# Optimization experiments

Hardware: AMD Instinct MI355X
Metric: run time of the kernel (lower is better)

The kernel has to match this reference:

```python
import jax, jax.numpy as jnp
import numpy as np

B, L, D, H, C, V, NC = 64, 64, 300, 128, 50, 50000, 2
LAMDA = 0.1
KS = (3, 4, 5)


def setup_inputs() -> dict:
    key = jax.random.key(0)
    ks = jax.random.split(key, 16)
    n = lambda k, shp, s=0.02: (jax.random.normal(k, shp, jnp.float32) * s)
    return {
        "x": jax.random.randint(ks[0], (B, L), 0, V),
        "embedmatrix": n(ks[1], (V, D), 0.1),
        "att_w1a": n(ks[2], (D, H)),      # first half of attlinear1 weight (for curembed)
        "att_w1b": n(ks[3], (D, H)),      # second half (for the paired embedding)
        "att_b1": jnp.zeros((H,), jnp.float32),
        "att_w2": n(ks[4], (H,)),
        "att_b2": jnp.zeros((), jnp.float32),
        "conv_w1": n(ks[5], (C, 2 * D, KS[0])), "conv_b1": jnp.zeros((C,), jnp.float32),
        "conv_w2": n(ks[6], (C, 2 * D, KS[1])), "conv_b2": jnp.zeros((C,), jnp.float32),
        "conv_w3": n(ks[7], (C, 2 * D, KS[2])), "conv_b3": jnp.zeros((C,), jnp.float32),
        "lin_w": n(ks[8], (3 * C, NC)), "lin_b": jnp.zeros((NC,), jnp.float32),
    }


def _attention(emb, w1a, w1b, b1, w2, b2):
    # Faithful vectorization of attentionembed/attentionword, including the
    # original's use of the COMPACTED index for the score partner and decay.
    Bb, Ll, Dd = emb.shape
    pa = emb @ w1a                        # [B,L,H]  curembed projection
    pb = emb[:, : Ll - 1] @ w1b           # [B,L-1,H] partner is outputs[:, index]
    h = jnp.tanh(pa[:, :, None, :] + pb[:, None, :, :] + b1)  # [B,L,L-1,H]
    s = h @ w2 + b2                       # [B,L,L-1]
    i = jnp.arange(Ll)[:, None]
    k = jnp.arange(Ll - 1)[None, :]
    decay = (1.0 - LAMDA) ** (jnp.abs(i - k) - 1).astype(jnp.float32)  # [L,L-1]
    alpha = jax.nn.softmax(decay * s, axis=-1)                         # [B,L,L-1]
    # attended embeddings use j = k + (k >= i) (skip position i)
    idx = k + (k >= i)                    # [L,L-1]
    alpha_full = jnp.zeros((Bb, Ll, Ll), emb.dtype).at[:, i, idx].set(alpha)
    return jnp.einsum('blm,bmd->bld', alpha_full, emb)  # [B,L,D]


def reference(x, embedmatrix, att_w1a, att_w1b, att_b1, att_w2, att_b2,
              conv_w1, conv_b1, conv_w2, conv_b2, conv_w3, conv_b3,
              lin_w, lin_b):
    emb = embedmatrix[x]                                   # [B,L,D]
    att = _attention(emb, att_w1a, att_w1b, att_b1, att_w2, att_b2)
    feat = jnp.concatenate([emb, att], axis=2).transpose(0, 2, 1)  # [B,2D,L]
    pooled = []
    for w, b in ((conv_w1, conv_b1), (conv_w2, conv_b2), (conv_w3, conv_b3)):
        y = jax.lax.conv_general_dilated(
            feat, w, window_strides=(1,), padding='VALID',
            dimension_numbers=('NCH', 'OIH', 'NCH')) + b[None, :, None]
        pooled.append(jnp.max(y, axis=-1))                 # pool over full valid length -> [B,C]
    conout = jnp.concatenate(pooled, axis=1)               # [B,3C]; dropout is identity in eval
    logits = conout @ lin_w + lin_b                        # [B,NC]
    return jax.nn.log_softmax(logits, axis=1)
```

## Files before the change

kernel.cpp:

```cpp
#include <hip/hip_runtime.h>
#include <math.h>

#define B_ 64
#define L_ 64
#define D_ 300
#define H_ 128
#define TWO_D 600
#define M_ 4096
#define Q_ 600
#define KP 640
#define KPA 320
#define HH 256

typedef short short8 __attribute__((ext_vector_type(8)));
typedef float floatx4 __attribute__((ext_vector_type(4)));

static __device__ __forceinline__ unsigned short f2bf(float f) {
    unsigned int u = __float_as_uint(f);
    u += 0x7FFFu + ((u >> 16) & 1u);
    return (unsigned short)(u >> 16);
}
static __device__ __forceinline__ float fast_tanh(float x) {
    float e = __expf(2.0f * x);
    return 1.0f - 2.0f * __builtin_amdgcn_rcpf(e + 1.0f);
}

__global__ __launch_bounds__(256) void k_prep(const int* __restrict__ x, const float* __restrict__ em,
        const float* __restrict__ w1a, const float* __restrict__ w1b,
        const float* __restrict__ cw1, const float* __restrict__ cw2, const float* __restrict__ cw3,
        unsigned short* __restrict__ fvb, unsigned short* __restrict__ wtT,
        unsigned short* __restrict__ w1abT) {
    int blk = blockIdx.x, tid = threadIdx.x;
    if (blk < 512) {
        #pragma unroll
        for (int r = 0; r < 8; ++r) {
            int m = blk * 8 + r;
            const float* src = em + (size_t)x[m] * D_;
            unsigned short* dst = fvb + (size_t)m * KP;
            for (int d = tid; d < KPA; d += 256) dst[d] = (d < D_) ? f2bf(src[d]) : 0;
            if (tid < 40) dst[TWO_D + tid] = 0;
        }
    } else if (blk < 912) {
        int base = ((blk - 512) * 256 + tid) * 4;
        #pragma unroll
        for (int e = 0; e < 4; ++e) {
            int idx = base + e;
            int q = idx / KP, d = idx - q * KP;
            float v = 0.f;
            if (q < Q_ && d < TWO_D) {
                if (q < 150)      { int c = q/3, i = q%3;                 v = cw1[((size_t)c*TWO_D + d)*3 + i]; }
                else if (q < 350) { int r2 = q-150; int c = r2/4, i = r2%4; v = cw2[((size_t)c*TWO_D + d)*4 + i]; }
                else              { int r2 = q-350; int c = r2/5, i = r2%5; v = cw3[((size_t)c*TWO_D + d)*5 + i]; }
            }
            wtT[idx] = f2bf(v);
        }
    } else {
        int base = ((blk - 912) * 256 + tid) * 4;
        #pragma unroll
        for (int e = 0; e < 4; ++e) {
            int idx = base + e;
            int h = idx / KPA, d = idx - h * KPA;
            float v = 0.f;
            if (d < D_) v = (h < H_) ? w1a[(size_t)d * H_ + h] : w1b[(size_t)d * H_ + (h - H_)];
            w1abT[idx] = f2bf(v);
        }
    }
}

__global__ __launch_bounds__(256) void k_papb(const unsigned short* __restrict__ A,
                                              const unsigned short* __restrict__ Bt,
                                              const float* __restrict__ b1,
                                              float* __restrict__ pab) {
    __shared__ unsigned short sA[64 * 72];
    __shared__ unsigned short sB[64 * 72];
    int m0 = blockIdx.x * 64, n0 = blockIdx.y * 64;
    int tid = threadIdx.x, lane = tid & 63, wave = tid >> 6;
    int wr = wave >> 1, wc = wave & 1;
    int sr = tid >> 2, so = (tid & 3) * 16;
    floatx4 acc[2][2] = {};
    int lr = lane & 15, lk = (lane >> 4) * 8;
    for (int k0 = 0; k0 < KPA; k0 += 64) {
        const unsigned short* Ar = &A [(size_t)(m0 + sr) * KP  + k0 + so];
        const unsigned short* Br = &Bt[(size_t)(n0 + sr) * KPA + k0 + so];
        *(uint4*)&sA[sr * 72 + so]     = *(const uint4*)Ar;
        *(uint4*)&sA[sr * 72 + so + 8] = *(const uint4*)(Ar + 8);
        *(uint4*)&sB[sr * 72 + so]     = *(const uint4*)Br;
        *(uint4*)&sB[sr * 72 + so + 8] = *(const uint4*)(Br + 8);
        __syncthreads();
        #pragma unroll
        for (int kk = 0; kk < 64; kk += 32) {
            short8 a0 = *(const short8*)&sA[(wr * 32 +  0 + lr) * 72 + kk + lk];
            short8 a1 = *(const short8*)&sA[(wr * 32 + 16 + lr) * 72 + kk + lk];
            short8 b0 = *(const short8*)&sB[(wc * 32 +  0 + lr) * 72 + kk + lk];
            short8 b1 = *(const short8*)&sB[(wc * 32 + 16 + lr) * 72 + kk + lk];
            acc[0][0] = __builtin_amdgcn_mfma_f32_16x16x32_bf16(a0, b0, acc[0][0], 0, 0, 0);
            acc[0][1] = __builtin_amdgcn_mfma_f32_16x16x32_bf16(a0, b1, acc[0][1], 0, 0, 0);
            acc[1][0] = __builtin_amdgcn_mfma_f32_16x16x32_bf16(a1, b0, acc[1][0], 0, 0, 0);
            acc[1][1] = __builtin_amdgcn_mfma_f32_16x16x32_bf16(a1, b1, acc[1][1], 0, 0, 0);
        }
        __syncthreads();
    }
    int drow = (lane >> 4) * 4, dcol = lane & 15;
    #pragma unroll
    for (int mi = 0; mi < 2; ++mi)
        #pragma unroll
        for (int ni = 0; ni < 2; ++ni) {
            int col = n0 + wc * 32 + ni * 16 + dcol;
            float bias = (col < H_) ? b1[col] : 0.f;
            #pragma unroll
            for (int i = 0; i < 4; ++i) {
                int row = m0 + wr * 32 + mi * 16 + drow + i;
                pab[(size_t)row * HH + col] = acc[mi][ni][i] + bias;
            }
        }
}

#define AT_PITCH 132
__global__ __launch_bounds__(256) void k_attn(const float* __restrict__ pab,
                                              const float* __restrict__ w2g,
                                              const float* __restrict__ b2,
                                              unsigned short* __restrict__ af) {
    int blk = blockIdx.x;
    int b = blk >> 2;
    int i0 = (blk & 3) * 16;
    __shared__ float pbL[64 * AT_PITCH];
    __shared__ float paL[16 * 128];
    __shared__ float s_w2[128];
    int tid = threadIdx.x, wave = tid >> 6, lane = tid & 63;
    {
        int r = tid >> 2, c0 = (tid & 3) * 32;
        #pragma unroll
        for (int c = 0; c < 32; c += 4) {
            float4 v = *(const float4*)&pab[(size_t)(b * 64 + r) * HH + H_ + c0 + c];
            *(float4*)&pbL[r * AT_PITCH + c0 + c] = v;
        }
    }
    {
        int idx = tid * 8;
        int ri = idx >> 7, h = idx & 127;
        const float* src = &pab[(size_t)(b * 64 + i0 + ri) * HH + h];
        *(float4*)&paL[idx]     = *(const float4*)src;
        *(float4*)&paL[idx + 4] = *(const float4*)(src + 4);
    }
    if (tid < 128) s_w2[tid] = w2g[tid];
    __syncthreads();

    float b2v = b2[0];
    int k = lane;
    float p0 = 0.f, p1 = 0.f, p2 = 0.f, p3 = 0.f;
    const float* pbrow = &pbL[k * AT_PITCH];
    const float* par = &paL[(wave * 4) * 128];
    for (int h = 0; h < 128; h += 4) {
        float4 pb4 = *(const float4*)&pbrow[h];
        float4 w4  = *(const float4*)&s_w2[h];
        float4 a0  = *(const float4*)&par[h];
        float4 a1  = *(const float4*)&par[128 + h];
        float4 a2  = *(const float4*)&par[256 + h];
        float4 a3  = *(const float4*)&par[384 + h];
        p0 += w4.x * fast_tanh(a0.x + pb4.x) + w4.y * fast_tanh(a0.y + pb4.y)
            + w4.z * fast_tanh(a0.z + pb4.z) + w4.w * fast_tanh(a0.w + pb4.w);
        p1 += w4.x * fast_tanh(a1.x + pb4.x) + w4.y * fast_tanh(a1.y + pb4.y)
            + w4.z * fast_tanh(a1.z + pb4.z) + w4.w * fast_tanh(a1.w + pb4.w);
        p2 += w4.x * fast_tanh(a2.x + pb4.x) + w4.y * fast_tanh(a2.y + pb4.y)
            + w4.z * fast_tanh(a2.z + pb4.z) + w4.w * fast_tanh(a2.w + pb4.w);
        p3 += w4.x * fast_tanh(a3.x + pb4.x) + w4.y * fast_tanh(a3.y + pb4.y)
            + w4.z * fast_tanh(a3.z + pb4.z) + w4.w * fast_tanh(a3.w + pb4.w);
    }
    #pragma unroll
    for (int j = 0; j < 4; ++j) {
        float p = (j == 0) ? p0 : (j == 1) ? p1 : (j == 2) ? p2 : p3;
        int i = i0 + wave * 4 + j;
        p += b2v;
        float v;
        if (k < 63) {
            float e = fabsf((float)(i - k)) - 1.0f;
            v = __expf(e * -0.10536051565782628f) * p;
        } else v = -INFINITY;
        float mx = v;
        #pragma unroll
        for (int off = 32; off; off >>= 1) mx = fmaxf(mx, __shfl_xor(mx, off, 64));
        float ex = (k < 63) ? __expf(v - mx) : 0.f;
        float sm = ex;
        #pragma unroll
        for (int off = 32; off; off >>= 1) sm += __shfl_xor(sm, off, 64);
        float alpha = ex * __builtin_amdgcn_rcpf(sm);
        int jj = (k < 63) ? (k + (k >= i)) : i;
        af[(size_t)(b * 64 + i) * 64 + jj] = (k < 63) ? f2bf(alpha) : (unsigned short)0;
    }
}

__global__ __launch_bounds__(256) void k_att_mfma(const unsigned short* __restrict__ af,
                                                  unsigned short* __restrict__ fvb) {
    int b = blockIdx.x;
    int n0 = blockIdx.y * 64;
    __shared__ unsigned short sA[64 * 72];
    __shared__ unsigned short sBt[64 * 72];
    int tid = threadIdx.x, wave = tid >> 6, lane = tid & 63;
    int sr = tid >> 2, so = (tid & 3) * 16;
    *(uint4*)&sA[sr * 72 + so]     = *(const uint4*)&af[(size_t)(b * 64 + sr) * 64 + so];
    *(uint4*)&sA[sr * 72 + so + 8] = *(const uint4*)&af[(size_t)(b * 64 + sr) * 64 + so + 8];
    int dg = n0 + lane;
    #pragma unroll
    for (int p = 0; p < 16; ++p) {
        int m = p * 4 + wave;
        unsigned short v = (dg < D_) ? fvb[(size_t)(b * 64 + m) * KP + dg] : (unsigned short)0;
        sBt[lane * 72 + m] = v;
    }
    __syncthreads();
    int wr = wave >> 1, wc = wave & 1;
    int lr = lane & 15, lk = (lane >> 4) * 8;
    floatx4 acc[2][2] = {};
    #pragma unroll
    for (int k0 = 0; k0 < 64; k0 += 32) {
        short8 a0 = *(const short8*)&sA [(wr * 32 +  0 + lr) * 72 + k0 + lk];
        short8 a1 = *(const short8*)&sA [(wr * 32 + 16 + lr) * 72 + k0 + lk];
        short8 b0 = *(const short8*)&sBt[(wc * 32 +  0 + lr) * 72 + k0 + lk];
        short8 b1 = *(const short8*)&sBt[(wc * 32 + 16 + lr) * 72 + k0 + lk];
        acc[0][0] = __builtin_amdgcn_mfma_f32_16x16x32_bf16(a0, b0, acc[0][0], 0, 0, 0);
        acc[0][1] = __builtin_amdgcn_mfma_f32_16x16x32_bf16(a0, b1, acc[0][1], 0, 0, 0);
        acc[1][0] = __builtin_amdgcn_mfma_f32_16x16x32_bf16(a1, b0, acc[1][0], 0, 0, 0);
        acc[1][1] = __builtin_amdgcn_mfma_f32_16x16x32_bf16(a1, b1, acc[1][1], 0, 0, 0);
    }
    int drow = (lane >> 4) * 4, dcol = lane & 15;
    #pragma unroll
    for (int mi = 0; mi < 2; ++mi)
        #pragma unroll
        for (int ni = 0; ni < 2; ++ni) {
            int dgo = n0 + wc * 32 + ni * 16 + dcol;
            if (dgo >= D_) continue;
            #pragma unroll
            for (int i = 0; i < 4; ++i) {
                int row = wr * 32 + mi * 16 + drow + i;
                fvb[(size_t)(b * 64 + row) * KP + D_ + dgo] = f2bf(acc[mi][ni][i]);
            }
        }
}

__global__ __launch_bounds__(256) void k_gemmT(const unsigned short* __restrict__ Wt,
                                               const unsigned short* __restrict__ Bv,
                                               float* __restrict__ GT) {
    __shared__ unsigned short sA[64 * 72];
    __shared__ unsigned short sB[64 * 72];
    int q0 = blockIdx.x * 64, n0 = blockIdx.y * 64;
    int tid = threadIdx.x, lane = tid & 63, wave = tid >> 6;
    int wr = wave >> 1, wc = wave & 1;
    int sr = tid >> 2, so = (tid & 3) * 16;
    floatx4 acc[2][2] = {};
    int lr = lane & 15, lk = (lane >> 4) * 8;
    for (int k0 = 0; k0 < KP; k0 += 64) {
        const unsigned short* Ar = &Wt[(size_t)(q0 + sr) * KP + k0 + so];
        const unsigned short* Br = &Bv[(size_t)(n0 + sr) * KP + k0 + so];
        *(uint4*)&sA[sr * 72 + so]     = *(const uint4*)Ar;
        *(uint4*)&sA[sr * 72 + so + 8] = *(const uint4*)(Ar + 8);
        *(uint4*)&sB[sr * 72 + so]     = *(const uint4*)Br;
        *(uint4*)&sB[sr * 72 + so + 8] = *(const uint4*)(Br + 8);
        __syncthreads();
        #pragma unroll
        for (int kk = 0; kk < 64; kk += 32) {
            short8 a0 = *(const short8*)&sA[(wr * 32 +  0 + lr) * 72 + kk + lk];
            short8 a1 = *(const short8*)&sA[(wr * 32 + 16 + lr) * 72 + kk + lk];
            short8 b0 = *(const short8*)&sB[(wc * 32 +  0 + lr) * 72 + kk + lk];
            short8 b1 = *(const short8*)&sB[(wc * 32 + 16 + lr) * 72 + kk + lk];
            acc[0][0] = __builtin_amdgcn_mfma_f32_16x16x32_bf16(a0, b0, acc[0][0], 0, 0, 0);
            acc[0][1] = __builtin_amdgcn_mfma_f32_16x16x32_bf16(a0, b1, acc[0][1], 0, 0, 0);
            acc[1][0] = __builtin_amdgcn_mfma_f32_16x16x32_bf16(a1, b0, acc[1][0], 0, 0, 0);
            acc[1][1] = __builtin_amdgcn_mfma_f32_16x16x32_bf16(a1, b1, acc[1][1], 0, 0, 0);
        }
        __syncthreads();
    }
    int drow = (lane >> 4) * 4, dcol = lane & 15;
    #pragma unroll
    for (int mi = 0; mi < 2; ++mi)
        #pragma unroll
        for (int ni = 0; ni < 2; ++ni) {
            int qrow = q0 + wr * 32 + mi * 16 + drow;
            int col  = n0 + wc * 32 + ni * 16 + dcol;
            #pragma unroll
            for (int i = 0; i < 4; ++i)
                GT[(size_t)(qrow + i) * M_ + col] = acc[mi][ni][i];
        }
}

__global__ __launch_bounds__(256) void k_pool(const float* __restrict__ GT,
        const float* __restrict__ cb1, const float* __restrict__ cb2, const float* __restrict__ cb3,
        float* __restrict__ conout) {
    int task = blockIdx.x * 4 + (threadIdx.x >> 6);
    int lane = threadIdx.x & 63;
    int b = task / 150, p = task - b * 150;
    int ks, qb; float bias;
    if (p < 50)       { ks = 3; qb = p * 3;              bias = cb1[p]; }
    else if (p < 100) { int c = p - 50;  ks = 4; qb = 150 + c * 4; bias = cb2[c]; }
    else              { int c = p - 100; ks = 5; qb = 350 + c * 5; bias = cb3[c]; }
    int T = L_ - ks + 1;
    float y = -INFINITY;
    if (lane < T) {
        float s = bias;
        for (int i = 0; i < ks; ++i)
            s += GT[(size_t)(qb + i) * M_ + b * 64 + lane + i];
        y = s;
    }
    #pragma unroll
    for (int off = 32; off; off >>= 1) y = fmaxf(y, __shfl_xor(y, off, 64));
    if (lane == 0) conout[b * 150 + p] = y;
}

__global__ void k_final(const float* __restrict__ conout, const float* __restrict__ lw,
                        const float* __restrict__ lb, float* __restrict__ out) {
    int b = threadIdx.x;
    if (b >= B_) return;
    float l0 = lb[0], l1 = lb[1];
    const float* co = conout + b * 150;
    for (int m = 0; m < 150; ++m) {
        float v = co[m];
        l0 += v * lw[m * 2 + 0];
        l1 += v * lw[m * 2 + 1];
    }
    float mx = fmaxf(l0, l1);
    float ls = mx + logf(expf(l0 - mx) + expf(l1 - mx));
    out[b * 2 + 0] = l0 - ls;
    out[b * 2 + 1] = l1 - ls;
}

extern "C" void kernel_launch(void* const* d_in, const int* in_sizes, int n_in,
                              void* d_out, int out_size, void* d_ws, size_t ws_size,
                              hipStream_t stream) {
    const int*   x   = (const int*)  d_in[0];
    const float* em  = (const float*)d_in[1];
    const float* w1a = (const float*)d_in[2];
    const float* w1b = (const float*)d_in[3];
    const float* b1  = (const float*)d_in[4];
    const float* w2  = (const float*)d_in[5];
    const float* b2  = (const float*)d_in[6];
    const float* cw1 = (const float*)d_in[7];
    const float* cb1 = (const float*)d_in[8];
    const float* cw2 = (const float*)d_in[9];
    const float* cb2 = (const float*)d_in[10];
    const float* cw3 = (const float*)d_in[11];
    const float* cb3 = (const float*)d_in[12];
    const float* lw  = (const float*)d_in[13];
    const float* lb  = (const float*)d_in[14];
    float* out = (float*)d_out;

    float* ws = (float*)d_ws;
    float*          GT     = ws;
    unsigned short* af     = (unsigned short*)ws;
    float*          pab    = ws + 2621440;
    unsigned short* fvb    = (unsigned short*)(ws + 3670016);
    unsigned short* WtT    = (unsigned short*)(ws + 4980736);
    unsigned short* w1abT  = (unsigned short*)(ws + 5185536);
    float*          conout = ws + 5226496;

    hipLaunchKernelGGL(k_prep, dim3(992), dim3(256), 0, stream,
                       x, em, w1a, w1b, cw1, cw2, cw3, fvb, WtT, w1abT);
    hipLaunchKernelGGL(k_papb, dim3(M_ / 64, HH / 64), dim3(256), 0, stream,
                       fvb, w1abT, b1, pab);
    hipLaunchKernelGGL(k_attn, dim3(256), dim3(256), 0, stream, pab, w2, b2, af);
    hipLaunchKernelGGL(k_att_mfma, dim3(B_, 5), dim3(256), 0, stream, af, fvb);
    hipLaunchKernelGGL(k_gemmT, dim3(KP / 64, M_ / 64), dim3(256), 0, stream,
                       WtT, fvb, GT);
    hipLaunchKernelGGL(k_pool, dim3(2400), dim3(256), 0, stream,
                       GT, cb1, cb2, cb3, conout);
    hipLaunchKernelGGL(k_final, dim3(1), dim3(64), 0, stream, conout, lw, lb, out);
}
```

Baseline: 61.80 us.

## Fuse pooling with final linear, widen gemm tile, double attention block threads

Three changes. The pool and final-linear kernels are merged into one kernel per batch that max-pools each conv channel and accumulates the two logits through shared memory, which drops a launch and the conout round-trip. The transposed conv GEMM now computes 64x128 tiles with 8 MFMA accumulators per wave, halving the grid and reusing each A fragment across more columns. The attention-score kernel runs 512 threads with 2 query rows per wave instead of 4, doubling waves per block at the cost of more block-level parallel overhead.

```diff
diff --git a/kernel.cpp b/kernel.cpp
--- a/kernel.cpp
+++ b/kernel.cpp
@@ -116,7 +116,7 @@
 }
 
 #define AT_PITCH 132
-__global__ __launch_bounds__(256) void k_attn(const float* __restrict__ pab,
+__global__ __launch_bounds__(512) void k_attn(const float* __restrict__ pab,
                                               const float* __restrict__ w2g,
                                               const float* __restrict__ b2,
                                               unsigned short* __restrict__ af) {
@@ -128,48 +128,40 @@
     __shared__ float s_w2[128];
     int tid = threadIdx.x, wave = tid >> 6, lane = tid & 63;
     {
-        int r = tid >> 2, c0 = (tid & 3) * 32;
-        #pragma unroll
-        for (int c = 0; c < 32; c += 4) {
+        int r = tid >> 3, c0 = (tid & 7) * 16;
+        #pragma unroll
+        for (int c = 0; c < 16; c += 4) {
             float4 v = *(const float4*)&pab[(size_t)(b * 64 + r) * HH + H_ + c0 + c];
             *(float4*)&pbL[r * AT_PITCH + c0 + c] = v;
         }
     }
     {
-        int idx = tid * 8;
+        int idx = tid * 4;
         int ri = idx >> 7, h = idx & 127;
-        const float* src = &pab[(size_t)(b * 64 + i0 + ri) * HH + h];
-        *(float4*)&paL[idx]     = *(const float4*)src;
-        *(float4*)&paL[idx + 4] = *(const float4*)(src + 4);
+        *(float4*)&paL[idx] = *(const float4*)&pab[(size_t)(b * 64 + i0 + ri) * HH + h];
     }
     if (tid < 128) s_w2[tid] = w2g[tid];
     __syncthreads();
 
     float b2v = b2[0];
     int k = lane;
-    float p0 = 0.f, p1 = 0.f, p2 = 0.f, p3 = 0.f;
+    float p0 = 0.f, p1 = 0.f;
     const float* pbrow = &pbL[k * AT_PITCH];
-    const float* par = &paL[(wave * 4) * 128];
+    const float* par = &paL[(wave * 2) * 128];
     for (int h = 0; h < 128; h += 4) {
         float4 pb4 = *(const float4*)&pbrow[h];
         float4 w4  = *(const float4*)&s_w2[h];
         float4 a0  = *(const float4*)&par[h];
         float4 a1  = *(const float4*)&par[128 + h];
-        float4 a2  = *(const float4*)&par[256 + h];
-        float4 a3  = *(const float4*)&par[384 + h];
         p0 += w4.x * fast_tanh(a0.x + pb4.x) + w4.y * fast_tanh(a0.y + pb4.y)
             + w4.z * fast_tanh(a0.z + pb4.z) + w4.w * fast_tanh(a0.w + pb4.w);
         p1 += w4.x * fast_tanh(a1.x + pb4.x) + w4.y * fast_tanh(a1.y + pb4.y)
             + w4.z * fast_tanh(a1.z + pb4.z) + w4.w * fast_tanh(a1.w + pb4.w);
-        p2 += w4.x * fast_tanh(a2.x + pb4.x) + w4.y * fast_tanh(a2.y + pb4.y)
-            + w4.z * fast_tanh(a2.z + pb4.z) + w4.w * fast_tanh(a2.w + pb4.w);
-        p3 += w4.x * fast_tanh(a3.x + pb4.x) + w4.y * fast_tanh(a3.y + pb4.y)
-            + w4.z * fast_tanh(a3.z + pb4.z) + w4.w * fast_tanh(a3.w + pb4.w);
-    }
-    #pragma unroll
-    for (int j = 0; j < 4; ++j) {
-        float p = (j == 0) ? p0 : (j == 1) ? p1 : (j == 2) ? p2 : p3;
-        int i = i0 + wave * 4 + j;
+    }
+    #pragma unroll
+    for (int j = 0; j < 2; ++j) {
+        float p = (j == 0) ? p0 : p1;
+        int i = i0 + wave * 2 + j;
         p += b2v;
         float v;
         if (k < 63) {
@@ -240,85 +232,90 @@
                                                const unsigned short* __restrict__ Bv,
                                                float* __restrict__ GT) {
     __shared__ unsigned short sA[64 * 72];
-    __shared__ unsigned short sB[64 * 72];
-    int q0 = blockIdx.x * 64, n0 = blockIdx.y * 64;
+    __shared__ unsigned short sB[128 * 72];
+    int q0 = blockIdx.x * 64, n0 = blockIdx.y * 128;
     int tid = threadIdx.x, lane = tid & 63, wave = tid >> 6;
-    int wr = wave >> 1, wc = wave & 1;
-    int sr = tid >> 2, so = (tid & 3) * 16;
-    floatx4 acc[2][2] = {};
+    int srA = tid >> 2, soA = (tid & 3) * 16;
+    int srB = tid >> 1, soB = (tid & 1) * 32;
+    floatx4 acc[4][2] = {};
     int lr = lane & 15, lk = (lane >> 4) * 8;
     for (int k0 = 0; k0 < KP; k0 += 64) {
-        const unsigned short* Ar = &Wt[(size_t)(q0 + sr) * KP + k0 + so];
-        const unsigned short* Br = &Bv[(size_t)(n0 + sr) * KP + k0 + so];
-        *(uint4*)&sA[sr * 72 + so]     = *(const uint4*)Ar;
-        *(uint4*)&sA[sr * 72 + so + 8] = *(const uint4*)(Ar + 8);
-        *(uint4*)&sB[sr * 72 + so]     = *(const uint4*)Br;
-        *(uint4*)&sB[sr * 72 + so + 8] = *(const uint4*)(Br + 8);
+        const unsigned short* Ar = &Wt[(size_t)(q0 + srA) * KP + k0 + soA];
+        *(uint4*)&sA[srA * 72 + soA]     = *(const uint4*)Ar;
+        *(uint4*)&sA[srA * 72 + soA + 8] = *(const uint4*)(Ar + 8);
+        const unsigned short* Br = &Bv[(size_t)(n0 + srB) * KP + k0 + soB];
+        *(uint4*)&sB[srB * 72 + soB]      = *(const uint4*)Br;
+        *(uint4*)&sB[srB * 72 + soB + 8]  = *(const uint4*)(Br + 8);
+        *(uint4*)&sB[srB * 72 + soB + 16] = *(const uint4*)(Br + 16);
+        *(uint4*)&sB[srB * 72 + soB + 24] = *(const uint4*)(Br + 24);
         __syncthreads();
         #pragma unroll
         for (int kk = 0; kk < 64; kk += 32) {
-            short8 a0 = *(const short8*)&sA[(wr * 32 +  0 + lr) * 72 + kk + lk];
-            short8 a1 = *(const short8*)&sA[(wr * 32 + 16 + lr) * 72 + kk + lk];
-            short8 b0 = *(const short8*)&sB[(wc * 32 +  0 + lr) * 72 + kk + lk];
-            short8 b1 = *(const short8*)&sB[(wc * 32 + 16 + lr) * 72 + kk + lk];
-            acc[0][0] = __builtin_amdgcn_mfma_f32_16x16x32_bf16(a0, b0, acc[0][0], 0, 0, 0);
-            acc[0][1] = __builtin_amdgcn_mfma_f32_16x16x32_bf16(a0, b1, acc[0][1], 0, 0, 0);
-            acc[1][0] = __builtin_amdgcn_mfma_f32_16x16x32_bf16(a1, b0, acc[1][0], 0, 0, 0);
-            acc[1][1] = __builtin_amdgcn_mfma_f32_16x16x32_bf16(a1, b1, acc[1][1], 0, 0, 0);
+            short8 aq[4], bm[2];
+            #pragma unroll
+            for (int qi = 0; qi < 4; ++qi)
+                aq[qi] = *(const short8*)&sA[(qi * 16 + lr) * 72 + kk + lk];
+            #pragma unroll
+            for (int mi = 0; mi < 2; ++mi)
+                bm[mi] = *(const short8*)&sB[(wave * 32 + mi * 16 + lr) * 72 + kk + lk];
+            #pragma unroll
+            for (int qi = 0; qi < 4; ++qi)
+                #pragma unroll
+                for (int mi = 0; mi < 2; ++mi)
+                    acc[qi][mi] = __builtin_amdgcn_mfma_f32_16x16x32_bf16(aq[qi], bm[mi], acc[qi][mi], 0, 0, 0);
         }
         __syncthreads();
     }
     int drow = (lane >> 4) * 4, dcol = lane & 15;
     #pragma unroll
-    for (int mi = 0; mi < 2; ++mi)
-        #pragma unroll
-        for (int ni = 0; ni < 2; ++ni) {
-            int qrow = q0 + wr * 32 + mi * 16 + drow;
-            int col  = n0 + wc * 32 + ni * 16 + dcol;
-            #pragma unroll
-            for (int i = 0; i < 4; ++i)
-                GT[(size_t)(qrow + i) * M_ + col] = acc[mi][ni][i];
-        }
-}
-
-__global__ __launch_bounds__(256) void k_pool(const float* __restrict__ GT,
+    for (int qi = 0; qi < 4; ++qi)
+        #pragma unroll
+        for (int mi = 0; mi < 2; ++mi) {
+            int col = n0 + wave * 32 + mi * 16 + dcol;
+            #pragma unroll
+            for (int i = 0; i < 4; ++i) {
+                int qr = q0 + qi * 16 + drow + i;
+                if (qr < Q_) GT[(size_t)qr * M_ + col] = acc[qi][mi][i];
+            }
+        }
+}
+
+__global__ __launch_bounds__(512) void k_poolfin(const float* __restrict__ GT,
         const float* __restrict__ cb1, const float* __restrict__ cb2, const float* __restrict__ cb3,
-        float* __restrict__ conout) {
-    int task = blockIdx.x * 4 + (threadIdx.x >> 6);
-    int lane = threadIdx.x & 63;
-    int b = task / 150, p = task - b * 150;
-    int ks, qb; float bias;
-    if (p < 50)       { ks = 3; qb = p * 3;              bias = cb1[p]; }
-    else if (p < 100) { int c = p - 50;  ks = 4; qb = 150 + c * 4; bias = cb2[c]; }
-    else              { int c = p - 100; ks = 5; qb = 350 + c * 5; bias = cb3[c]; }
-    int T = L_ - ks + 1;
-    float y = -INFINITY;
-    if (lane < T) {
-        float s = bias;
-        for (int i = 0; i < ks; ++i)
-            s += GT[(size_t)(qb + i) * M_ + b * 64 + lane + i];
-        y = s;
-    }
-    #pragma unroll
-    for (int off = 32; off; off >>= 1) y = fmaxf(y, __shfl_xor(y, off, 64));
-    if (lane == 0) conout[b * 150 + p] = y;
-}
-
-__global__ void k_final(const float* __restrict__ conout, const float* __restrict__ lw,
-                        const float* __restrict__ lb, float* __restrict__ out) {
-    int b = threadIdx.x;
-    if (b >= B_) return;
-    float l0 = lb[0], l1 = lb[1];
-    const float* co = conout + b * 150;
-    for (int m = 0; m < 150; ++m) {
-        float v = co[m];
-        l0 += v * lw[m * 2 + 0];
-        l1 += v * lw[m * 2 + 1];
-    }
-    float mx = fmaxf(l0, l1);
-    float ls = mx + logf(expf(l0 - mx) + expf(l1 - mx));
-    out[b * 2 + 0] = l0 - ls;
-    out[b * 2 + 1] = l1 - ls;
+        const float* __restrict__ lw, const float* __restrict__ lb, float* __restrict__ out) {
+    int b = blockIdx.x;
+    int tid = threadIdx.x, wave = tid >> 6, lane = tid & 63;
+    __shared__ float part[8][2];
+    float l0 = 0.f, l1 = 0.f;
+    for (int p = wave; p < 150; p += 8) {
+        int ks, qb; float bias;
+        if (p < 50)       { ks = 3; qb = p * 3;              bias = cb1[p]; }
+        else if (p < 100) { int c = p - 50;  ks = 4; qb = 150 + c * 4; bias = cb2[c]; }
+        else              { int c = p - 100; ks = 5; qb = 350 + c * 5; bias = cb3[c]; }
+        int T = L_ - ks + 1;
+        float y = -INFINITY;
+        if (lane < T) {
+            float s = bias;
+            for (int i = 0; i < ks; ++i)
+                s += GT[(size_t)(qb + i) * M_ + b * 64 + lane + i];
+            y = s;
+        }
+        #pragma unroll
+        for (int off = 32; off; off >>= 1) y = fmaxf(y, __shfl_xor(y, off, 64));
+        l0 += y * lw[p * 2 + 0];
+        l1 += y * lw[p * 2 + 1];
+    }
+    if (lane == 0) { part[wave][0] = l0; part[wave][1] = l1; }
+    __syncthreads();
+    if (tid == 0) {
+        float s0 = lb[0], s1 = lb[1];
+        #pragma unroll
+        for (int w = 0; w < 8; ++w) { s0 += part[w][0]; s1 += part[w][1]; }
+        float mx = fmaxf(s0, s1);
+        float ls = mx + logf(expf(s0 - mx) + expf(s1 - mx));
+        out[b * 2 + 0] = s0 - ls;
+        out[b * 2 + 1] = s1 - ls;
+    }
 }
 
 extern "C" void kernel_launch(void* const* d_in, const int* in_sizes, int n_in,
@@ -348,17 +345,15 @@
     unsigned short* fvb    = (unsigned short*)(ws + 3670016);
     unsigned short* WtT    = (unsigned short*)(ws + 4980736);
     unsigned short* w1abT  = (unsigned short*)(ws + 5185536);
-    float*          conout = ws + 5226496;
 
     hipLaunchKernelGGL(k_prep, dim3(992), dim3(256), 0, stream,
                        x, em, w1a, w1b, cw1, cw2, cw3, fvb, WtT, w1abT);
     hipLaunchKernelGGL(k_papb, dim3(M_ / 64, HH / 64), dim3(256), 0, stream,
                        fvb, w1abT, b1, pab);
-    hipLaunchKernelGGL(k_attn, dim3(256), dim3(256), 0, stream, pab, w2, b2, af);
+    hipLaunchKernelGGL(k_attn, dim3(256), dim3(512), 0, stream, pab, w2, b2, af);
     hipLaunchKernelGGL(k_att_mfma, dim3(B_, 5), dim3(256), 0, stream, af, fvb);
-    hipLaunchKernelGGL(k_gemmT, dim3(KP / 64, M_ / 64), dim3(256), 0, stream,
+    hipLaunchKernelGGL(k_gemmT, dim3(KP / 64, M_ / 128), dim3(256), 0, stream,
                        WtT, fvb, GT);
-    hipLaunchKernelGGL(k_pool, dim3(2400), dim3(256), 0, stream,
-                       GT, cb1, cb2, cb3, conout);
-    hipLaunchKernelGGL(k_final, dim3(1), dim3(64), 0, stream, conout, lw, lb, out);
-}
+    hipLaunchKernelGGL(k_poolfin, dim3(B_), dim3(512), 0, stream,
+                       GT, cb1, cb2, cb3, lw, lb, out);
+}
```

Measured after the change: 78.58 us. 1.27x slower.
